# Kernel optimization log

Measured on AMD Instinct MI355X. Metric: run time of the kernel, lower is better.

Reference implementation:

```python
import jax, jax.numpy as jnp
import numpy as np

# Model dims
N = 4096      # tokens (batch 2 * seq 2048, flattened)
D = 1024      # d_model
E = 16        # num_expert
K = 2         # top_k
H = 2048      # expert hidden dim
CAP = 1024


def setup_inputs() -> dict:
    key = jax.random.key(0)
    k0, k1, k2, k3 = jax.random.split(key, 4)
    s_d = 1.0 / np.sqrt(D).astype(np.float32)
    s_h = 1.0 / np.sqrt(H).astype(np.float32)
    return {
        "moe_inp": jax.random.normal(k0, (N, D), jnp.float32),
        "Wg": jax.random.normal(k1, (D, E), jnp.float32) * s_d,   # NaiveGate linear
        "bg": jnp.zeros((E,), jnp.float32),
        "W1": jax.random.normal(k2, (E, D, H), jnp.float32) * s_d,  # per-expert FFN layer 1
        "b1": jnp.zeros((E, H), jnp.float32),
        "W2": jax.random.normal(k3, (E, H, D), jnp.float32) * s_h,  # per-expert FFN layer 2
        "b2": jnp.zeros((E, D), jnp.float32),
    }


def reference(moe_inp, Wg, bg, W1, b1, W2, b2):
    # ---- gate (NaiveGate): linear -> top_k -> softmax over selected logits ----
    logits = moe_inp @ Wg + bg                      # [N, E]
    top_v, top_i = jax.lax.top_k(logits, K)         # [N, K]
    gate_score = jax.nn.softmax(top_v, axis=-1)     # [N, K]

    # ---- dispatch (MOEScatter): sort tokens into contiguous per-expert buffers ----
    flat_e = top_i.reshape(-1)                      # [N*K] expert id per assignment
    oh = jax.nn.one_hot(flat_e, E, dtype=jnp.int32)               # [N*K, E]
    pos_all = jnp.cumsum(oh, axis=0) - oh                          # rank within expert
    pos = jnp.take_along_axis(pos_all, flat_e[:, None], axis=1)[:, 0]  # [N*K]
    valid = pos < CAP
    pos_safe = jnp.where(valid, pos, CAP)           # out-of-range -> dropped by scatter

    x_rep = jnp.repeat(moe_inp, K, axis=0)          # [N*K, D]
    x_e = jnp.zeros((E, CAP, D), moe_inp.dtype).at[flat_e, pos_safe].set(
        x_rep, mode='drop')                          # [E, CAP, D]

    # ---- per-expert grouped FFN (expert_fn) ----
    h = jax.nn.gelu(jnp.einsum('ecd,edh->ech', x_e, W1) + b1[:, None, :])  # [E, CAP, H]
    y_e = jnp.einsum('ech,ehd->ecd', h, W2) + b2[:, None, :]               # [E, CAP, D]

    # ---- gather (MOEGather) + weighted combine by gate scores ----
    y_tok = y_e.at[flat_e, pos_safe].get(mode='fill', fill_value=0.0)      # [N*K, D]
    y_tok = y_tok * valid[:, None].astype(y_tok.dtype)
    y = y_tok.reshape(N, K, D)
    return jnp.einsum('nkd,nk->nd', y, gate_score)  # [N, D]
```

## Files before the change

kernel.cpp:

```cpp
#include <hip/hip_runtime.h>

#define N_TOK 4096
#define DMODEL 1024
#define NEXP 16
#define HDIM 2048
#define CAP 1024

typedef __attribute__((ext_vector_type(8))) short frag8;
typedef __attribute__((ext_vector_type(4))) float f32x4;
typedef __attribute__((ext_vector_type(8))) unsigned short us8;

__device__ __forceinline__ unsigned short f2bf(float x) {
  unsigned u = __builtin_bit_cast(unsigned, x);
  u += 0x7fffu + ((u >> 16) & 1u);
  return (unsigned short)(u >> 16);
}
__device__ __forceinline__ float bf2f(unsigned short b) {
  unsigned u = ((unsigned)b) << 16;
  return __builtin_bit_cast(float, u);
}
__device__ __forceinline__ void load_lds16(const void* g, void* l) {
  __builtin_amdgcn_global_load_lds((const __attribute__((address_space(1))) void*)g,
                                   (__attribute__((address_space(3))) void*)l, 16, 0, 0);
}
#define SBAR0 __builtin_amdgcn_sched_barrier(0)

__global__ __launch_bounds__(256) void gate_logits_kernel(
    const float* __restrict__ x, const float* __restrict__ Wg, const float* __restrict__ bg,
    int* __restrict__ a_e, float* __restrict__ a_gate)
{
  int wid = threadIdx.x >> 6, l = threadIdx.x & 63;
  int n = blockIdx.x * 4 + wid;
  const float* xr = x + (size_t)n * DMODEL;
  float acc[NEXP];
#pragma unroll
  for (int e = 0; e < NEXP; ++e) acc[e] = 0.f;
#pragma unroll
  for (int q = 0; q < 4; ++q) {
    float4 xv = *(const float4*)(xr + q * 256 + l * 4);
    const float* wr = Wg + (size_t)(q * 256 + l * 4) * NEXP;
#pragma unroll
    for (int j = 0; j < 4; ++j) {
      float xs = j == 0 ? xv.x : j == 1 ? xv.y : j == 2 ? xv.z : xv.w;
      const float4* w4 = (const float4*)(wr + j * NEXP);
#pragma unroll
      for (int qq = 0; qq < 4; ++qq) {
        float4 w = w4[qq];
        acc[qq*4+0] += xs * w.x; acc[qq*4+1] += xs * w.y;
        acc[qq*4+2] += xs * w.z; acc[qq*4+3] += xs * w.w;
      }
    }
  }
#pragma unroll
  for (int e = 0; e < NEXP; ++e) {
    float v = acc[e];
#pragma unroll
    for (int off = 32; off > 0; off >>= 1) v += __shfl_xor(v, off, 64);
    acc[e] = v + bg[e];
  }
  if (l == 0) {
    int i1 = 0; float v1 = acc[0];
#pragma unroll
    for (int e = 1; e < NEXP; ++e) if (acc[e] > v1) { v1 = acc[e]; i1 = e; }
    int i2 = -1; float v2 = -1e30f;
#pragma unroll
    for (int e = 0; e < NEXP; ++e) if (e != i1 && acc[e] > v2) { v2 = acc[e]; i2 = e; }
    float e2 = __expf(v2 - v1);
    float inv = 1.f / (1.f + e2);
    a_e[n*2] = i1;   a_gate[n*2] = inv;
    a_e[n*2+1] = i2; a_gate[n*2+1] = e2 * inv;
  }
}

__global__ __launch_bounds__(256) void assign_kernel(
    const int* __restrict__ a_e, int* __restrict__ a_slot,
    int* __restrict__ tok_of_slot, int* __restrict__ cnt)
{
  __shared__ int c;
  if (threadIdx.x == 0) c = 0;
  __syncthreads();
  int eid = blockIdx.x;
  for (int j = threadIdx.x; j < N_TOK * 2; j += 256) {
    if (a_e[j] == eid) {
      int p = atomicAdd(&c, 1);
      a_slot[j] = p;
      if (p < CAP) tok_of_slot[eid * CAP + p] = j >> 1;
    }
  }
  __syncthreads();
  if (threadIdx.x == 0) cnt[eid] = c;
}

__global__ __launch_bounds__(256) void gather_kernel(
    const float* __restrict__ x, const int* __restrict__ cnt,
    const int* __restrict__ tok_of_slot, unsigned short* __restrict__ Xe)
{
  int rid = blockIdx.x * 2 + (threadIdx.x >> 7);
  int tl = threadIdx.x & 127;
  int e = rid >> 10, slot = rid & (CAP - 1);
  int c = cnt[e]; if (c > CAP) c = CAP;
  if (slot >= c) return;
  int tok = tok_of_slot[rid];
  const float4* xs = (const float4*)(x + (size_t)tok * DMODEL + tl * 8);
  float4 u = xs[0], v = xs[1];
  us8 p;
  p[0]=f2bf(u.x); p[1]=f2bf(u.y); p[2]=f2bf(u.z); p[3]=f2bf(u.w);
  p[4]=f2bf(v.x); p[5]=f2bf(v.y); p[6]=f2bf(v.z); p[7]=f2bf(v.w);
  int kt = tl >> 3, s = tl & 7;
  int row = slot & 127, rt = slot >> 7;
  size_t off = ((size_t)((e*8 + rt)*16 + kt)) * 8192 + (size_t)row*64 + ((s ^ (row & 7)) << 3);
  *(us8*)&Xe[off] = p;
}

template<int KT, int NT, bool GELU, bool OUT_BLOCKED>
__global__ __launch_bounds__(256, 3) void gemm_kernel(
    const unsigned short* __restrict__ Aimg, const float* __restrict__ W,
    unsigned short* __restrict__ OutU, const float* __restrict__ bias,
    const int* __restrict__ cnt)
{
  constexpr int LDW = NT * 128;
  __shared__ __align__(16) char smem[49152];
  constexpr int NBLK = NEXP * 8 * NT;
  int bid = blockIdx.x;
  int item = (bid & 7) * (NBLK / 8) + (bid >> 3);
  int e = item / (8 * NT), rem = item % (8 * NT);
  int mt = rem / NT, nt = rem % NT;
  int mcnt = cnt[e]; if (mcnt > CAP) mcnt = CAP;
  if (mt * 128 >= mcnt) return;
  int t = threadIdx.x, l = t & 63, wid = t >> 6;
  int wm = wid >> 1, wn = wid & 1;
  int rA = l & 15, g = l >> 4, r7 = rA & 7;
  int sw0 = (g ^ r7) << 4, sw1 = ((g + 4) ^ r7) << 4;

  const char* asrc = (const char*)(Aimg + (size_t)(e * 8 + mt) * KT * 8192);
  int brow = t & 127;
  int bk0 = (t >> 7) * 32;
  int bs0 = bk0 >> 3;
  int bsig = brow & 7;
  const float* wsrc = W + (size_t)e * (KT * 64) * LDW + (size_t)nt * 128 + brow;
  float br[32];

  auto loadB = [&](int kt) {
    const float* p = wsrc + (size_t)(kt * 64 + bk0) * LDW;
#pragma unroll
    for (int j = 0; j < 32; ++j) br[j] = p[(size_t)j * LDW];
  };
  auto writeB = [&]() {
    char* lB = smem + 32768;
#pragma unroll
    for (int c2 = 0; c2 < 4; ++c2) {
      us8 p8;
#pragma unroll
      for (int j = 0; j < 8; ++j) p8[j] = f2bf(br[c2 * 8 + j]);
      *(us8*)(lB + brow * 128 + (((bs0 + c2) ^ bsig) << 4)) = p8;
    }
  };
  auto stageA = [&](char* dst, int kt) {
    const char* s = asrc + (size_t)kt * 16384;
    load_lds16(s + t * 16,         dst + t * 16);
    load_lds16(s + 4096 + t * 16,  dst + 4096 + t * 16);
    load_lds16(s + 8192 + t * 16,  dst + 8192 + t * 16);
    load_lds16(s + 12288 + t * 16, dst + 12288 + t * 16);
  };

  f32x4 acc[4][4] = {};
  char* A0 = smem;
  char* A1 = smem + 16384;

  auto compute = [&](const char* aBuf) {
    const char* bA = aBuf + (wm * 64 + rA) * 128;
    const char* bB = smem + 32768 + (wn * 64 + rA) * 128;
    frag8 bfr[4][2];
#pragma unroll
    for (int n16 = 0; n16 < 4; ++n16) {
      bfr[n16][0] = *(const frag8*)(bB + n16 * 2048 + sw0);
      bfr[n16][1] = *(const frag8*)(bB + n16 * 2048 + sw1);
    }
    __builtin_amdgcn_s_setprio(1);
#pragma unroll
    for (int m16 = 0; m16 < 4; ++m16) {
      frag8 a0 = *(const frag8*)(bA + m16 * 2048 + sw0);
      frag8 a1 = *(const frag8*)(bA + m16 * 2048 + sw1);
#pragma unroll
      for (int n16 = 0; n16 < 4; ++n16) {
        acc[m16][n16] = __builtin_amdgcn_mfma_f32_16x16x32_bf16(a0, bfr[n16][0], acc[m16][n16], 0, 0, 0);
        acc[m16][n16] = __builtin_amdgcn_mfma_f32_16x16x32_bf16(a1, bfr[n16][1], acc[m16][n16], 0, 0, 0);
      }
    }
    __builtin_amdgcn_s_setprio(0);
  };

  loadB(0); SBAR0;
  stageA(A0, 0); SBAR0;
  asm volatile("s_waitcnt vmcnt(4)" ::: "memory");
  writeB();
  loadB(1); SBAR0;
  stageA(A1, 1); SBAR0;
  asm volatile("s_waitcnt vmcnt(36)" ::: "memory");
  asm volatile("s_waitcnt lgkmcnt(0)" ::: "memory");
  SBAR0; __builtin_amdgcn_s_barrier(); SBAR0;

  int cur = 0;
  for (int kt = 0; kt < KT; ++kt) {
    compute(cur ? A1 : A0);
    if (kt + 1 < KT) {
      asm volatile("s_waitcnt vmcnt(4)" ::: "memory");
      SBAR0; __builtin_amdgcn_s_barrier(); SBAR0;
      writeB();
      int k2 = (kt + 2 < KT) ? kt + 2 : KT - 1;
      loadB(k2); SBAR0;
      stageA(cur ? A1 : A0, k2); SBAR0;
      asm volatile("s_waitcnt vmcnt(36)" ::: "memory");
      asm volatile("s_waitcnt lgkmcnt(0)" ::: "memory");
      SBAR0; __builtin_amdgcn_s_barrier(); SBAR0;
      cur ^= 1;
    }
  }
  asm volatile("s_waitcnt vmcnt(0)" ::: "memory");
  asm volatile("s_waitcnt lgkmcnt(0)" ::: "memory");
  SBAR0; __builtin_amdgcn_s_barrier(); SBAR0;

  float bv[4];
#pragma unroll
  for (int n16 = 0; n16 < 4; ++n16)
    bv[n16] = bias[e * LDW + nt * 128 + wn * 64 + n16 * 16 + rA];

  char* wb = smem + wid * 8192;
  if constexpr (OUT_BLOCKED) {
#pragma unroll
    for (int m16 = 0; m16 < 4; ++m16)
#pragma unroll
      for (int n16 = 0; n16 < 4; ++n16)
#pragma unroll
        for (int rr = 0; rr < 4; ++rr) {
          float xv = acc[m16][n16][rr] + bv[n16];
          if (GELU) {
            float u = 0.7978845608028654f * (xv + 0.044715f * xv * xv * xv);
            xv = xv / (1.f + __expf(-2.f * u));
          }
          int row = m16 * 16 + g * 4 + rr;
          int col = n16 * 16 + rA;
          *(unsigned short*)(wb + row * 128 + (((col >> 3) ^ (row & 7)) << 4) + (col & 7) * 2) = f2bf(xv);
        }
    asm volatile("s_waitcnt lgkmcnt(0)" ::: "memory");
    size_t ob = ((size_t)(e * 8 + mt) * (2 * NT) + nt * 2 + wn) * 8192;
#pragma unroll
    for (int it = 0; it < 8; ++it) {
      int row = it * 8 + (l >> 3), p = l & 7;
      us8 v = *(const us8*)(wb + row * 128 + p * 16);
      *(us8*)&OutU[ob + (size_t)(wm * 64 + row) * 64 + p * 8] = v;
    }
  } else {
#pragma unroll
    for (int m16 = 0; m16 < 4; ++m16)
#pragma unroll
      for (int n16 = 0; n16 < 4; ++n16)
#pragma unroll
        for (int rr = 0; rr < 4; ++rr) {
          int row = m16 * 16 + g * 4 + rr;
          int col = n16 * 16 + rA;
          *(unsigned short*)(wb + row * 128 + col * 2) = f2bf(acc[m16][n16][rr] + bv[n16]);
        }
    asm volatile("s_waitcnt lgkmcnt(0)" ::: "memory");
#pragma unroll
    for (int it = 0; it < 8; ++it) {
      int row = it * 8 + (l >> 3), p = l & 7;
      us8 v = *(const us8*)(wb + row * 128 + p * 16);
      *(us8*)&OutU[(size_t)(e * CAP + mt * 128 + wm * 64 + row) * LDW
                   + nt * 128 + wn * 64 + p * 8] = v;
    }
  }
}

__global__ __launch_bounds__(256) void combine_kernel(
    const unsigned short* __restrict__ ye, const int* __restrict__ a_e,
    const int* __restrict__ a_slot, const float* __restrict__ a_gate, float* __restrict__ out)
{
  int n = blockIdx.x, t = threadIdx.x;
  int e0 = a_e[n*2], e1 = a_e[n*2+1];
  int s0 = a_slot[n*2], s1 = a_slot[n*2+1];
  float g0 = a_gate[n*2], g1 = a_gate[n*2+1];
  float r[4] = {0.f, 0.f, 0.f, 0.f};
  if (s0 < CAP) {
    ushort4 v = *(const ushort4*)&ye[(size_t)(e0*CAP + s0)*DMODEL + t*4];
    r[0] += g0*bf2f(v.x); r[1] += g0*bf2f(v.y); r[2] += g0*bf2f(v.z); r[3] += g0*bf2f(v.w);
  }
  if (s1 < CAP) {
    ushort4 v = *(const ushort4*)&ye[(size_t)(e1*CAP + s1)*DMODEL + t*4];
    r[0] += g1*bf2f(v.x); r[1] += g1*bf2f(v.y); r[2] += g1*bf2f(v.z); r[3] += g1*bf2f(v.w);
  }
  float4 o; o.x = r[0]; o.y = r[1]; o.z = r[2]; o.w = r[3];
  *(float4*)&out[(size_t)n*DMODEL + t*4] = o;
}

extern "C" void kernel_launch(void* const* d_in, const int* in_sizes, int n_in,
                              void* d_out, int out_size, void* d_ws, size_t ws_size,
                              hipStream_t stream) {
  const float* x  = (const float*)d_in[0];
  const float* Wg = (const float*)d_in[1];
  const float* bg = (const float*)d_in[2];
  const float* W1 = (const float*)d_in[3];
  const float* b1 = (const float*)d_in[4];
  const float* W2 = (const float*)d_in[5];
  const float* b2 = (const float*)d_in[6];
  float* out = (float*)d_out;
  char* ws = (char*)d_ws;

  unsigned short* Xe = (unsigned short*)(ws);
  unsigned short* hB = (unsigned short*)(ws + 33554432);
  unsigned short* ye = (unsigned short*)(ws + 100663296);
  int* cnt           = (int*)(ws + 134217728);
  int* tok           = (int*)(ws + 134217792);
  int* a_e           = (int*)(ws + 134283328);
  int* a_slot        = (int*)(ws + 134316096);
  float* a_gate      = (float*)(ws + 134348864);

  gate_logits_kernel<<<1024, 256, 0, stream>>>(x, Wg, bg, a_e, a_gate);
  assign_kernel<<<16, 256, 0, stream>>>(a_e, a_slot, tok, cnt);
  gather_kernel<<<8192, 256, 0, stream>>>(x, cnt, tok, Xe);
  gemm_kernel<16, 16, true,  true ><<<2048, 256, 0, stream>>>(Xe, W1, hB, b1, cnt);
  gemm_kernel<32, 8,  false, false><<<1024, 256, 0, stream>>>(hB, W2, ye, b2, cnt);
  combine_kernel<<<4096, 256, 0, stream>>>(ye, a_e, a_slot, a_gate, out);
}
```

Baseline: 227.8 us.

## Enlarge grouped GEMM M-tile to 256 rows to halve fp32 weight reloads

```diff
diff --git a/kernel.cpp b/kernel.cpp
--- a/kernel.cpp
+++ b/kernel.cpp
@@ -113,26 +113,29 @@
 }
 
 template<int KT, int NT, bool GELU, bool OUT_BLOCKED>
-__global__ __launch_bounds__(256, 3) void gemm_kernel(
+__global__ __launch_bounds__(256, 2) void gemm_kernel(
     const unsigned short* __restrict__ Aimg, const float* __restrict__ W,
     unsigned short* __restrict__ OutU, const float* __restrict__ bias,
     const int* __restrict__ cnt)
 {
   constexpr int LDW = NT * 128;
-  __shared__ __align__(16) char smem[49152];
-  constexpr int NBLK = NEXP * 8 * NT;
+  __shared__ __align__(16) char smem[81920];
+  constexpr int NBLK = NEXP * 4 * NT;
   int bid = blockIdx.x;
   int item = (bid & 7) * (NBLK / 8) + (bid >> 3);
-  int e = item / (8 * NT), rem = item % (8 * NT);
-  int mt = rem / NT, nt = rem % NT;
+  int e = item / (4 * NT), rem = item % (4 * NT);
+  int st = rem >> 4, r3 = rem & 15;
+  int mtp = r3 >> 2;
+  int nt  = st * 4 + (r3 & 3);
   int mcnt = cnt[e]; if (mcnt > CAP) mcnt = CAP;
-  if (mt * 128 >= mcnt) return;
+  if (mtp * 256 >= mcnt) return;
   int t = threadIdx.x, l = t & 63, wid = t >> 6;
   int wm = wid >> 1, wn = wid & 1;
   int rA = l & 15, g = l >> 4, r7 = rA & 7;
   int sw0 = (g ^ r7) << 4, sw1 = ((g + 4) ^ r7) << 4;
 
-  const char* asrc = (const char*)(Aimg + (size_t)(e * 8 + mt) * KT * 8192);
+  const char* asrc0 = (const char*)(Aimg + (size_t)(e * 8 + mtp * 2 + 0) * KT * 8192);
+  const char* asrc1 = (const char*)(Aimg + (size_t)(e * 8 + mtp * 2 + 1) * KT * 8192);
   int brow = t & 127;
   int bk0 = (t >> 7) * 32;
   int bs0 = bk0 >> 3;
@@ -146,7 +149,7 @@
     for (int j = 0; j < 32; ++j) br[j] = p[(size_t)j * LDW];
   };
   auto writeB = [&]() {
-    char* lB = smem + 32768;
+    char* lB = smem + 65536;
 #pragma unroll
     for (int c2 = 0; c2 < 4; ++c2) {
       us8 p8;
@@ -156,20 +159,25 @@
     }
   };
   auto stageA = [&](char* dst, int kt) {
-    const char* s = asrc + (size_t)kt * 16384;
-    load_lds16(s + t * 16,         dst + t * 16);
-    load_lds16(s + 4096 + t * 16,  dst + 4096 + t * 16);
-    load_lds16(s + 8192 + t * 16,  dst + 8192 + t * 16);
-    load_lds16(s + 12288 + t * 16, dst + 12288 + t * 16);
+    const char* s0 = asrc0 + (size_t)kt * 16384;
+    const char* s1 = asrc1 + (size_t)kt * 16384;
+    load_lds16(s0 + t * 16,         dst + t * 16);
+    load_lds16(s0 + 4096 + t * 16,  dst + 4096 + t * 16);
+    load_lds16(s0 + 8192 + t * 16,  dst + 8192 + t * 16);
+    load_lds16(s0 + 12288 + t * 16, dst + 12288 + t * 16);
+    load_lds16(s1 + t * 16,         dst + 16384 + t * 16);
+    load_lds16(s1 + 4096 + t * 16,  dst + 20480 + t * 16);
+    load_lds16(s1 + 8192 + t * 16,  dst + 24576 + t * 16);
+    load_lds16(s1 + 12288 + t * 16, dst + 28672 + t * 16);
   };
 
-  f32x4 acc[4][4] = {};
+  f32x4 acc[8][4] = {};
   char* A0 = smem;
-  char* A1 = smem + 16384;
+  char* A1 = smem + 32768;
 
   auto compute = [&](const char* aBuf) {
-    const char* bA = aBuf + (wm * 64 + rA) * 128;
-    const char* bB = smem + 32768 + (wn * 64 + rA) * 128;
+    const char* bA = aBuf + wm * 16384 + rA * 128;
+    const char* bB = smem + 65536 + (wn * 64 + rA) * 128;
     frag8 bfr[4][2];
 #pragma unroll
     for (int n16 = 0; n16 < 4; ++n16) {
@@ -178,7 +186,7 @@
     }
     __builtin_amdgcn_s_setprio(1);
 #pragma unroll
-    for (int m16 = 0; m16 < 4; ++m16) {
+    for (int m16 = 0; m16 < 8; ++m16) {
       frag8 a0 = *(const frag8*)(bA + m16 * 2048 + sw0);
       frag8 a1 = *(const frag8*)(bA + m16 * 2048 + sw1);
 #pragma unroll
@@ -192,11 +200,11 @@
 
   loadB(0); SBAR0;
   stageA(A0, 0); SBAR0;
-  asm volatile("s_waitcnt vmcnt(4)" ::: "memory");
+  asm volatile("s_waitcnt vmcnt(8)" ::: "memory");
   writeB();
   loadB(1); SBAR0;
   stageA(A1, 1); SBAR0;
-  asm volatile("s_waitcnt vmcnt(36)" ::: "memory");
+  asm volatile("s_waitcnt vmcnt(40)" ::: "memory");
   asm volatile("s_waitcnt lgkmcnt(0)" ::: "memory");
   SBAR0; __builtin_amdgcn_s_barrier(); SBAR0;
 
@@ -204,13 +212,13 @@
   for (int kt = 0; kt < KT; ++kt) {
     compute(cur ? A1 : A0);
     if (kt + 1 < KT) {
-      asm volatile("s_waitcnt vmcnt(4)" ::: "memory");
+      asm volatile("s_waitcnt vmcnt(8)" ::: "memory");
       SBAR0; __builtin_amdgcn_s_barrier(); SBAR0;
       writeB();
       int k2 = (kt + 2 < KT) ? kt + 2 : KT - 1;
       loadB(k2); SBAR0;
       stageA(cur ? A1 : A0, k2); SBAR0;
-      asm volatile("s_waitcnt vmcnt(36)" ::: "memory");
+      asm volatile("s_waitcnt vmcnt(40)" ::: "memory");
       asm volatile("s_waitcnt lgkmcnt(0)" ::: "memory");
       SBAR0; __builtin_amdgcn_s_barrier(); SBAR0;
       cur ^= 1;
@@ -225,10 +233,10 @@
   for (int n16 = 0; n16 < 4; ++n16)
     bv[n16] = bias[e * LDW + nt * 128 + wn * 64 + n16 * 16 + rA];
 
-  char* wb = smem + wid * 8192;
+  char* wb = smem + wid * 16384;
   if constexpr (OUT_BLOCKED) {
 #pragma unroll
-    for (int m16 = 0; m16 < 4; ++m16)
+    for (int m16 = 0; m16 < 8; ++m16)
 #pragma unroll
       for (int n16 = 0; n16 < 4; ++n16)
 #pragma unroll
@@ -243,16 +251,16 @@
           *(unsigned short*)(wb + row * 128 + (((col >> 3) ^ (row & 7)) << 4) + (col & 7) * 2) = f2bf(xv);
         }
     asm volatile("s_waitcnt lgkmcnt(0)" ::: "memory");
-    size_t ob = ((size_t)(e * 8 + mt) * (2 * NT) + nt * 2 + wn) * 8192;
-#pragma unroll
-    for (int it = 0; it < 8; ++it) {
+    size_t ob = ((size_t)(e * 8 + mtp * 2 + wm) * (2 * NT) + nt * 2 + wn) * 8192;
+#pragma unroll
+    for (int it = 0; it < 16; ++it) {
       int row = it * 8 + (l >> 3), p = l & 7;
       us8 v = *(const us8*)(wb + row * 128 + p * 16);
-      *(us8*)&OutU[ob + (size_t)(wm * 64 + row) * 64 + p * 8] = v;
+      *(us8*)&OutU[ob + (size_t)row * 64 + p * 8] = v;
     }
   } else {
 #pragma unroll
-    for (int m16 = 0; m16 < 4; ++m16)
+    for (int m16 = 0; m16 < 8; ++m16)
 #pragma unroll
       for (int n16 = 0; n16 < 4; ++n16)
 #pragma unroll
@@ -263,10 +271,10 @@
         }
     asm volatile("s_waitcnt lgkmcnt(0)" ::: "memory");
 #pragma unroll
-    for (int it = 0; it < 8; ++it) {
+    for (int it = 0; it < 16; ++it) {
       int row = it * 8 + (l >> 3), p = l & 7;
       us8 v = *(const us8*)(wb + row * 128 + p * 16);
-      *(us8*)&OutU[(size_t)(e * CAP + mt * 128 + wm * 64 + row) * LDW
+      *(us8*)&OutU[(size_t)(e * CAP + mtp * 256 + wm * 128 + row) * LDW
                    + nt * 128 + wn * 64 + p * 8] = v;
     }
   }
@@ -318,7 +326,7 @@
   gate_logits_kernel<<<1024, 256, 0, stream>>>(x, Wg, bg, a_e, a_gate);
   assign_kernel<<<16, 256, 0, stream>>>(a_e, a_slot, tok, cnt);
   gather_kernel<<<8192, 256, 0, stream>>>(x, cnt, tok, Xe);
-  gemm_kernel<16, 16, true,  true ><<<2048, 256, 0, stream>>>(Xe, W1, hB, b1, cnt);
-  gemm_kernel<32, 8,  false, false><<<1024, 256, 0, stream>>>(hB, W2, ye, b2, cnt);
+  gemm_kernel<16, 16, true,  true ><<<1024, 256, 0, stream>>>(Xe, W1, hB, b1, cnt);
+  gemm_kernel<32, 8,  false, false><<<512, 256, 0, stream>>>(hB, W2, ye, b2, cnt);
   combine_kernel<<<4096, 256, 0, stream>>>(ye, a_e, a_slot, a_gate, out);
 }
```

After: 242.0 us. 6.2% more time.
